# Kernel tuning notes

Measured on AMD Instinct MI355X. Metric: run time of the kernel, lower is better.

The kernel has to match this reference:

```python
import jax, jax.numpy as jnp
import numpy as np

N = 100000
IN_DIM = 128
OUT_DIM = 128
HEADS = 4
C = OUT_DIM // HEADS  # per-head channels = 32
E = 1600000
EPS = 1e-5
NEG_SLOPE = 0.2


def setup_inputs() -> dict:
    key = jax.random.key(0)
    ks = jax.random.split(key, 10)
    prev = jax.random.normal(ks[0], (N, OUT_DIM), dtype=jnp.float32)
    x = jax.random.normal(ks[1], (N, IN_DIM), dtype=jnp.float32)
    edge_index = jax.random.randint(ks[2], (2, E), 0, N, dtype=jnp.int32)
    # GATConv parameters (glorot-ish scale)
    W = jax.random.normal(ks[3], (IN_DIM, HEADS * C), dtype=jnp.float32) * (1.0 / np.sqrt(IN_DIM))
    att_src = jax.random.normal(ks[4], (HEADS, C), dtype=jnp.float32) * (1.0 / np.sqrt(C))
    att_dst = jax.random.normal(ks[5], (HEADS, C), dtype=jnp.float32) * (1.0 / np.sqrt(C))
    bias = jnp.zeros((HEADS * C,), dtype=jnp.float32)
    # BatchNorm1d affine params
    gamma = jnp.ones((OUT_DIM,), dtype=jnp.float32)
    beta = jnp.zeros((OUT_DIM,), dtype=jnp.float32)
    return {"prev": prev, "x": x, "edge_index": edge_index, "W": W,
            "att_src": att_src, "att_dst": att_dst, "bias": bias,
            "gamma": gamma, "beta": beta}


def reference(prev, x, edge_index, W, att_src, att_dst, bias, gamma, beta):
    # --- GATConv (PyG defaults: add_self_loops=True, concat=True, neg_slope=0.2) ---
    n = x.shape[0]
    # add self loops
    loops = jnp.arange(n, dtype=edge_index.dtype)
    src = jnp.concatenate([edge_index[0], loops])  # [E+N] message source j
    dst = jnp.concatenate([edge_index[1], loops])  # [E+N] message target i

    h = (x @ W).reshape(n, HEADS, C)               # [N,H,C]
    a_src = jnp.einsum('nhc,hc->nh', h, att_src)   # [N,H]
    a_dst = jnp.einsum('nhc,hc->nh', h, att_dst)   # [N,H]

    alpha = a_src[src] + a_dst[dst]                # [E',H]
    alpha = jax.nn.leaky_relu(alpha, NEG_SLOPE)
    # segment softmax over incoming edges of each dst node
    amax = jax.ops.segment_max(alpha, dst, num_segments=n)       # [N,H]
    alpha = jnp.exp(alpha - amax[dst])
    asum = jax.ops.segment_sum(alpha, dst, num_segments=n)       # [N,H]
    alpha = alpha / asum[dst]

    msg = h[src] * alpha[:, :, None]                              # [E',H,C]
    out = jax.ops.segment_sum(msg, dst, num_segments=n)          # [N,H,C]
    out = out.reshape(n, HEADS * C) + bias                       # concat heads + bias

    # --- residual + BatchNorm1d (training-mode batch stats) + activation ---
    y = prev + out
    mean = jnp.mean(y, axis=0)
    var = jnp.mean(jnp.square(y - mean), axis=0)  # biased variance (torch BN)
    y = gamma * (y - mean) * jax.lax.rsqrt(var + EPS) + beta
    return jax.nn.relu(y)
```

## Files before the change

kernel.cpp:

```cpp
#include <hip/hip_runtime.h>
#include <math.h>

#define DIM 128
#define NEG 0.2f
#define EPS 1e-5f
#define LOG2E 1.4426950408889634f

#if __has_builtin(__builtin_amdgcn_exp2f)
#define EXP2(x) __builtin_amdgcn_exp2f(x)
#else
#define EXP2(x) exp2f(x)
#endif

typedef __attribute__((ext_vector_type(8))) short short8v;
typedef __attribute__((ext_vector_type(4))) float f32x4;

static __device__ __forceinline__ float leaky(float a) { return a > 0.f ? a : NEG * a; }
static __device__ __forceinline__ float bf2f(unsigned short u) {
    return __uint_as_float(((unsigned int)u) << 16);
}
static __device__ __forceinline__ unsigned short f2bf(float f) {
    unsigned int u = __float_as_uint(f);
    unsigned int r = (u + 0x7fffu + ((u >> 16) & 1u)) >> 16;
    return (unsigned short)r;
}

__global__ __launch_bounds__(256) void k_gemm(const float* __restrict__ x,
                                              const float* __restrict__ W,
                                              const float* __restrict__ att_s,
                                              const float* __restrict__ att_d,
                                              unsigned int* __restrict__ hpk,
                                              float* __restrict__ asrc,
                                              float* __restrict__ adst, int n) {
    __shared__ __align__(16) unsigned short xs[16][136];
    const int tid = threadIdx.x;
    const int w = tid >> 6;
    const int lane = tid & 63;
    const int lm = lane & 15;
    const int lk = lane >> 4;
    short8v bfrag[2][4];
#pragma unroll
    for (int ct = 0; ct < 2; ++ct) {
        int c = w * 32 + ct * 16 + lm;
#pragma unroll
        for (int q = 0; q < 4; ++q) {
            short8v f;
#pragma unroll
            for (int j = 0; j < 8; ++j) {
                int k = q * 32 + lk * 8 + j;
                f[j] = (short)f2bf(W[k * DIM + c]);
            }
            bfrag[ct][q] = f;
        }
    }
    const float asv0 = att_s[w * 32 + lm] * LOG2E;
    const float asv1 = att_s[w * 32 + 16 + lm] * LOG2E;
    const float adv0 = att_d[w * 32 + lm] * LOG2E;
    const float adv1 = att_d[w * 32 + 16 + lm] * LOG2E;

    const int nchunk = (n + 15) >> 4;
    for (int chunk = blockIdx.x; chunk < nchunk; chunk += gridDim.x) {
        const int r0 = chunk * 16;
        {
            int row = tid >> 4;
            int c8 = (tid & 15) * 8;
            int rg = min(r0 + row, n - 1);
            const float4* xp = (const float4*)(x + (size_t)rg * DIM + c8);
            float4 v0 = xp[0], v1 = xp[1];
            short8v t;
            t[0] = (short)f2bf(v0.x); t[1] = (short)f2bf(v0.y);
            t[2] = (short)f2bf(v0.z); t[3] = (short)f2bf(v0.w);
            t[4] = (short)f2bf(v1.x); t[5] = (short)f2bf(v1.y);
            t[6] = (short)f2bf(v1.z); t[7] = (short)f2bf(v1.w);
            *(short8v*)(&xs[row][c8]) = t;
        }
        __syncthreads();
        f32x4 acc0 = {0.f, 0.f, 0.f, 0.f}, acc1 = {0.f, 0.f, 0.f, 0.f};
#pragma unroll
        for (int q = 0; q < 4; ++q) {
            short8v a = *(const short8v*)(&xs[lm][q * 32 + lk * 8]);
            acc0 = __builtin_amdgcn_mfma_f32_16x16x32_bf16(a, bfrag[0][q], acc0, 0, 0, 0);
            acc1 = __builtin_amdgcn_mfma_f32_16x16x32_bf16(a, bfrag[1][q], acc1, 0, 0, 0);
        }
        __syncthreads();
        float ps[4], qs[4];
#pragma unroll
        for (int j = 0; j < 4; ++j) {
            ps[j] = acc0[j] * asv0 + acc1[j] * asv1;
            qs[j] = acc0[j] * adv0 + acc1[j] * adv1;
        }
#pragma unroll
        for (int m = 1; m < 16; m <<= 1) {
#pragma unroll
            for (int j = 0; j < 4; ++j) {
                ps[j] += __shfl_xor(ps[j], m);
                qs[j] += __shfl_xor(qs[j], m);
            }
        }
#pragma unroll
        for (int j = 0; j < 4; ++j) {
            int r = r0 + 4 * lk + j;
            if (r < n) {
                hpk[(size_t)r * 64 + 16 * w + lm] =
                    (unsigned int)f2bf(acc0[j]) | ((unsigned int)f2bf(acc1[j]) << 16);
                if (lm == 0) {
                    asrc[r * 4 + w] = ps[j];
                    adst[r * 4 + w] = qs[j];
                }
            }
        }
    }
}

__global__ void k_init(int* __restrict__ deg, float* __restrict__ stats, int n) {
    int t = blockIdx.x * blockDim.x + threadIdx.x;
    if (t < n) deg[t] = 1;
    if (t < 256) stats[t] = 0.f;
}

__global__ __launch_bounds__(256) void k_hist(const int* __restrict__ dst,
                                              int* __restrict__ deg, int E, int n) {
    const int g = blockIdx.x & 7;
    const int gb = blockIdx.x >> 3;
    const int nblk = gridDim.x >> 3;
    const int wsz = (n + 7) >> 3;
    const int lo = g * wsz;
    const int hi = min(lo + wsz, n);
    const int step = nblk * 256;
    for (int t = gb * 256 + threadIdx.x; t < E; t += step) {
        int d = dst[t];
        if (d >= lo && d < hi) atomicAdd(&deg[d], 1);
    }
}

__global__ __launch_bounds__(256) void k_scan_part(const int* __restrict__ deg,
                                                   int* __restrict__ bsum, int n) {
    int idx = blockIdx.x * 1024 + threadIdx.x * 4;
    int4 v = {0, 0, 0, 0};
    if (idx + 3 < n) v = *(const int4*)(deg + idx);
    else {
        if (idx + 0 < n) v.x = deg[idx + 0];
        if (idx + 1 < n) v.y = deg[idx + 1];
        if (idx + 2 < n) v.z = deg[idx + 2];
    }
    int s = v.x + v.y + v.z + v.w;
#pragma unroll
    for (int m = 1; m < 64; m <<= 1) s += __shfl_xor(s, m);
    __shared__ int ws[4];
    if ((threadIdx.x & 63) == 0) ws[threadIdx.x >> 6] = s;
    __syncthreads();
    if (threadIdx.x == 0) bsum[blockIdx.x] = ws[0] + ws[1] + ws[2] + ws[3];
}

__global__ __launch_bounds__(256) void k_scan_tops(int* __restrict__ bsum, int B) {
    __shared__ int lds[256];
    int t = threadIdx.x;
    int v = (t < B) ? bsum[t] : 0;
    lds[t] = v;
    __syncthreads();
    int acc = v;
    for (int ofs = 1; ofs < 256; ofs <<= 1) {
        int u = (t >= ofs) ? lds[t - ofs] : 0;
        __syncthreads();
        acc += u;
        lds[t] = acc;
        __syncthreads();
    }
    if (t < B) bsum[t] = acc - v;
}

__global__ __launch_bounds__(256) void k_scan_add(const int* __restrict__ deg,
                                                  const int* __restrict__ bsum,
                                                  int* __restrict__ row_start,
                                                  int* __restrict__ cursor, int n, int total) {
    int t = threadIdx.x;
    int idx = blockIdx.x * 1024 + t * 4;
    int4 v = {0, 0, 0, 0};
    if (idx + 3 < n) v = *(const int4*)(deg + idx);
    else {
        if (idx + 0 < n) v.x = deg[idx + 0];
        if (idx + 1 < n) v.y = deg[idx + 1];
        if (idx + 2 < n) v.z = deg[idx + 2];
    }
    int s = v.x + v.y + v.z + v.w;
    __shared__ int lds[256];
    lds[t] = s;
    __syncthreads();
    int acc = s;
    for (int ofs = 1; ofs < 256; ofs <<= 1) {
        int u = (t >= ofs) ? lds[t - ofs] : 0;
        __syncthreads();
        acc += u;
        lds[t] = acc;
        __syncthreads();
    }
    int excl = bsum[blockIdx.x] + acc - s;
    int4 rs;
    rs.x = excl;
    rs.y = rs.x + v.x;
    rs.z = rs.y + v.y;
    rs.w = rs.z + v.z;
    if (idx + 3 < n) {
        *(int4*)(row_start + idx) = rs;
        *(int4*)(cursor + idx) = rs;
    } else {
        if (idx + 0 < n) { row_start[idx + 0] = rs.x; cursor[idx + 0] = rs.x; }
        if (idx + 1 < n) { row_start[idx + 1] = rs.y; cursor[idx + 1] = rs.y; }
        if (idx + 2 < n) { row_start[idx + 2] = rs.z; cursor[idx + 2] = rs.z; }
    }
    if (blockIdx.x == 0 && t == 0) row_start[n] = total;
}

__global__ __launch_bounds__(256) void k_scatter(const int* __restrict__ src,
                                                 const int* __restrict__ dst,
                                                 const float4* __restrict__ asrc4,
                                                 const float4* __restrict__ adst4,
                                                 int* __restrict__ cursor,
                                                 int* __restrict__ csr,
                                                 uint2* __restrict__ pw,
                                                 int E, int n) {
    const int g = blockIdx.x & 7;
    const int gb = blockIdx.x >> 3;
    const int nblk = gridDim.x >> 3;
    const int wsz = (n + 7) >> 3;
    const int lo = g * wsz;
    const int hi = min(lo + wsz, n);
    const int total = E + n;
    const int step = nblk * 256;
    for (int t = gb * 256 + threadIdx.x; t < total; t += step) {
        int d, sv;
        if (t < E) {
            d = dst[t];
            sv = src[t];
        } else {
            d = t - E;
            sv = d;
        }
        if (d >= lo && d < hi) {
            float4 a = asrc4[sv];
            float4 b = adst4[d];
            float p0 = EXP2(leaky(a.x + b.x));
            float p1 = EXP2(leaky(a.y + b.y));
            float p2 = EXP2(leaky(a.z + b.z));
            float p3 = EXP2(leaky(a.w + b.w));
            int slot = atomicAdd(&cursor[d], 1);
            csr[slot] = sv;
            uint2 o;
            o.x = (unsigned int)f2bf(p0) | ((unsigned int)f2bf(p1) << 16);
            o.y = (unsigned int)f2bf(p2) | ((unsigned int)f2bf(p3) << 16);
            pw[slot] = o;
        }
    }
}

__global__ __launch_bounds__(256) void k_agg(const unsigned int* __restrict__ hw,
                                             const unsigned short* __restrict__ pwh,
                                             const int* __restrict__ row_start,
                                             const int* __restrict__ csr,
                                             const float* __restrict__ prev,
                                             const float* __restrict__ bias,
                                             float* __restrict__ ypre,
                                             float* __restrict__ stats, int n) {
    const int lane = threadIdx.x & 63;
    const int hd = lane >> 4;
    const int ch = 32 * hd + (lane & 15);
    int wave = blockIdx.x * 4 + (threadIdx.x >> 6);
    int nw = gridDim.x * 4;
    const float bb0 = bias[ch], bb1 = bias[ch + 16];
    float bsum0 = 0.f, bsq0 = 0.f, bsum1 = 0.f, bsq1 = 0.f;
    for (int i0 = wave; i0 < n; i0 += nw) {
        int i = __builtin_amdgcn_readfirstlane(i0);
        int e0 = row_start[i], e1 = row_start[i + 1];
        float s = 0.f, acc0 = 0.f, acc1 = 0.f;
        for (int e = e0; e < e1; e += 16) {
            int j[16];
            float p[16];
            unsigned int hp[16];
#pragma unroll
            for (int r = 0; r < 16; ++r) {
                int ec = min(e + r, e1 - 1);
                j[r] = csr[ec];
                p[r] = bf2f(pwh[ec * 4 + hd]);
            }
#pragma unroll
            for (int r = 0; r < 16; ++r) hp[r] = hw[(size_t)j[r] * 64 + lane];
#pragma unroll
            for (int r = 0; r < 16; ++r) {
                float pp = (e + r < e1) ? p[r] : 0.f;
                s += pp;
                acc0 = fmaf(pp, __uint_as_float(hp[r] << 16), acc0);
                acc1 = fmaf(pp, __uint_as_float(hp[r] & 0xffff0000u), acc1);
            }
        }
        float rs = 1.0f / s;
        size_t base = (size_t)i * DIM;
        float o0 = fmaf(acc0, rs, bb0 + prev[base + ch]);
        float o1 = fmaf(acc1, rs, bb1 + prev[base + ch + 16]);
        ypre[base + ch] = o0;
        ypre[base + ch + 16] = o1;
        bsum0 += o0; bsq0 = fmaf(o0, o0, bsq0);
        bsum1 += o1; bsq1 = fmaf(o1, o1, bsq1);
    }
    __shared__ float red[4][256];
    red[0][threadIdx.x] = bsum0;
    red[1][threadIdx.x] = bsq0;
    red[2][threadIdx.x] = bsum1;
    red[3][threadIdx.x] = bsq1;
    __syncthreads();
    if (threadIdx.x < 64) {
        int t = threadIdx.x;
        int c = 32 * (t >> 4) + (t & 15);
        float v0 = red[0][t] + red[0][t + 64] + red[0][t + 128] + red[0][t + 192];
        float v1 = red[1][t] + red[1][t + 64] + red[1][t + 128] + red[1][t + 192];
        float v2 = red[2][t] + red[2][t + 64] + red[2][t + 128] + red[2][t + 192];
        float v3 = red[3][t] + red[3][t + 64] + red[3][t + 128] + red[3][t + 192];
        atomicAdd(&stats[c], v0);
        atomicAdd(&stats[c + 16], v2);
        atomicAdd(&stats[128 + c], v1);
        atomicAdd(&stats[128 + c + 16], v3);
    }
}

__global__ void k_bnfin(const float* __restrict__ stats, const float* __restrict__ gamma,
                        const float* __restrict__ beta, float* __restrict__ AB, int n) {
    int c = threadIdx.x;
    float fn = (float)n;
    float mean = stats[c] / fn;
    float var = stats[128 + c] / fn - mean * mean;
    float a = gamma[c] * rsqrtf(var + EPS);
    AB[c] = a;
    AB[128 + c] = beta[c] - mean * a;
}

__global__ __launch_bounds__(256) void k_final(float* __restrict__ y,
                                               const float* __restrict__ AB, int total4) {
    int t0 = blockIdx.x * blockDim.x + threadIdx.x;
    int stride = gridDim.x * blockDim.x;
    for (int t = t0; t < total4; t += stride) {
        float4 v = ((float4*)y)[t];
        int c0 = (t * 4) & 127;
        v.x = fmaf(v.x, AB[c0 + 0], AB[128 + c0 + 0]);
        v.y = fmaf(v.y, AB[c0 + 1], AB[128 + c0 + 1]);
        v.z = fmaf(v.z, AB[c0 + 2], AB[128 + c0 + 2]);
        v.w = fmaf(v.w, AB[c0 + 3], AB[128 + c0 + 3]);
        v.x = v.x > 0.f ? v.x : 0.f;
        v.y = v.y > 0.f ? v.y : 0.f;
        v.z = v.z > 0.f ? v.z : 0.f;
        v.w = v.w > 0.f ? v.w : 0.f;
        ((float4*)y)[t] = v;
    }
}

extern "C" void kernel_launch(void* const* d_in, const int* in_sizes, int n_in,
                              void* d_out, int out_size, void* d_ws, size_t ws_size,
                              hipStream_t stream) {
    const float* prev  = (const float*)d_in[0];
    const float* x     = (const float*)d_in[1];
    const int*   ei    = (const int*)d_in[2];
    const float* W     = (const float*)d_in[3];
    const float* att_s = (const float*)d_in[4];
    const float* att_d = (const float*)d_in[5];
    const float* bias  = (const float*)d_in[6];
    const float* gamma = (const float*)d_in[7];
    const float* beta  = (const float*)d_in[8];
    const int n = in_sizes[0] / DIM;
    const int E = in_sizes[2] / 2;
    const int* src = ei;
    const int* dst = ei + E;

    char* p = (char*)d_ws;
    auto alloc = [&](size_t bytes) {
        void* q = (void*)p;
        p += (bytes + 255) & ~(size_t)255;
        return q;
    };
    unsigned int* hpk = (unsigned int*)alloc((size_t)n * 64 * 4);
    float* asrc      = (float*)alloc((size_t)n * 4 * 4);
    float* adst      = (float*)alloc((size_t)n * 4 * 4);
    int*   deg       = (int*)alloc((size_t)(n + 1) * 4);
    int*   row_start = (int*)alloc((size_t)(n + 1) * 4);
    int*   cursor    = (int*)alloc((size_t)(n + 1) * 4);
    int*   csr       = (int*)alloc((size_t)(E + n + 16) * 4);
    uint2* pw        = (uint2*)alloc((size_t)(E + n + 16) * 8);
    int*   bsum      = (int*)alloc(1024 * 4);
    float* stats     = (float*)alloc(256 * 4);
    float* AB        = (float*)alloc(256 * 4);
    float* yout      = (float*)d_out;

    int B = (n + 1023) / 1024;
    k_init<<<dim3((n + 255) / 256), dim3(256), 0, stream>>>(deg, stats, n);
    k_gemm<<<dim3(1024), dim3(256), 0, stream>>>(x, W, att_s, att_d, hpk, asrc, adst, n);
    k_hist<<<dim3(2048), dim3(256), 0, stream>>>(dst, deg, E, n);
    k_scan_part<<<dim3(B), dim3(256), 0, stream>>>(deg, bsum, n);
    k_scan_tops<<<dim3(1), dim3(256), 0, stream>>>(bsum, B);
    k_scan_add<<<dim3(B), dim3(256), 0, stream>>>(deg, bsum, row_start, cursor, n, E + n);
    k_scatter<<<dim3(2048), dim3(256), 0, stream>>>(src, dst, (const float4*)asrc,
                                                    (const float4*)adst, cursor, csr, pw, E, n);
    k_agg<<<dim3(2048), dim3(256), 0, stream>>>(hpk, (const unsigned short*)pw, row_start,
                                                csr, prev, bias, yout, stats, n);
    k_bnfin<<<dim3(1), dim3(128), 0, stream>>>(stats, gamma, beta, AB, n);
    int total4 = n * DIM / 4;
    k_final<<<dim3(2048), dim3(256), 0, stream>>>(yout, AB, total4);
}
```

Baseline: 307.3 us.

## Gather neighbor rows with 16-byte loads, four edges per wave step

The aggregation kernel now splits each wave into four quarter-waves that each handle a different edge. Each lane loads a uint4 holding eight bf16 channels of the neighbor row, where before every lane loaded one 4-byte word per edge. The goal is fewer, wider gather instructions and more edges in flight per load batch. In exchange it adds a cross-quarter shuffle reduction per node, leaves three quarters of the lanes idle during the output epilogue, and changes the BN stats reduction layout.

```diff
diff --git a/kernel.cpp b/kernel.cpp
--- a/kernel.cpp
+++ b/kernel.cpp
@@ -262,62 +262,89 @@
                                              float* __restrict__ ypre,
                                              float* __restrict__ stats, int n) {
     const int lane = threadIdx.x & 63;
-    const int hd = lane >> 4;
-    const int ch = 32 * hd + (lane & 15);
-    int wave = blockIdx.x * 4 + (threadIdx.x >> 6);
+    const int ql = lane >> 4;
+    const int ll = lane & 15;
+    const int hq = ll >> 2;
+    const int wv = threadIdx.x >> 6;
+    int wave = blockIdx.x * 4 + wv;
     int nw = gridDim.x * 4;
-    const float bb0 = bias[ch], bb1 = bias[ch + 16];
-    float bsum0 = 0.f, bsq0 = 0.f, bsum1 = 0.f, bsq1 = 0.f;
-    for (int i0 = wave; i0 < n; i0 += nw) {
-        int i = __builtin_amdgcn_readfirstlane(i0);
+    float bs_lo[4] = {0.f, 0.f, 0.f, 0.f}, bq_lo[4] = {0.f, 0.f, 0.f, 0.f};
+    float bs_hi[4] = {0.f, 0.f, 0.f, 0.f}, bq_hi[4] = {0.f, 0.f, 0.f, 0.f};
+    for (int i = wave; i < n; i += nw) {
         int e0 = row_start[i], e1 = row_start[i + 1];
-        float s = 0.f, acc0 = 0.f, acc1 = 0.f;
+        float s = 0.f;
+        float ac_lo[4] = {0.f, 0.f, 0.f, 0.f}, ac_hi[4] = {0.f, 0.f, 0.f, 0.f};
         for (int e = e0; e < e1; e += 16) {
-            int j[16];
-            float p[16];
-            unsigned int hp[16];
-#pragma unroll
-            for (int r = 0; r < 16; ++r) {
-                int ec = min(e + r, e1 - 1);
-                j[r] = csr[ec];
-                p[r] = bf2f(pwh[ec * 4 + hd]);
-            }
-#pragma unroll
-            for (int r = 0; r < 16; ++r) hp[r] = hw[(size_t)j[r] * 64 + lane];
-#pragma unroll
-            for (int r = 0; r < 16; ++r) {
-                float pp = (e + r < e1) ? p[r] : 0.f;
-                s += pp;
-                acc0 = fmaf(pp, __uint_as_float(hp[r] << 16), acc0);
-                acc1 = fmaf(pp, __uint_as_float(hp[r] & 0xffff0000u), acc1);
-            }
-        }
-        float rs = 1.0f / s;
-        size_t base = (size_t)i * DIM;
-        float o0 = fmaf(acc0, rs, bb0 + prev[base + ch]);
-        float o1 = fmaf(acc1, rs, bb1 + prev[base + ch + 16]);
-        ypre[base + ch] = o0;
-        ypre[base + ch + 16] = o1;
-        bsum0 += o0; bsq0 = fmaf(o0, o0, bsq0);
-        bsum1 += o1; bsq1 = fmaf(o1, o1, bsq1);
-    }
-    __shared__ float red[4][256];
-    red[0][threadIdx.x] = bsum0;
-    red[1][threadIdx.x] = bsq0;
-    red[2][threadIdx.x] = bsum1;
-    red[3][threadIdx.x] = bsq1;
+            int j[4];
+            float pp[4];
+            uint4 hv[4];
+#pragma unroll
+            for (int b = 0; b < 4; ++b) {
+                int ee = e + b * 4 + ql;
+                int ec = min(ee, e1 - 1);
+                j[b] = csr[ec];
+                pp[b] = (ee < e1) ? bf2f(pwh[ec * 4 + hq]) : 0.f;
+            }
+#pragma unroll
+            for (int b = 0; b < 4; ++b)
+                hv[b] = ((const uint4*)(hw + (size_t)j[b] * 64))[ll];
+#pragma unroll
+            for (int b = 0; b < 4; ++b) {
+                s += pp[b];
+                unsigned int h0 = hv[b].x, h1 = hv[b].y, h2 = hv[b].z, h3 = hv[b].w;
+                ac_lo[0] = fmaf(pp[b], __uint_as_float(h0 << 16), ac_lo[0]);
+                ac_hi[0] = fmaf(pp[b], __uint_as_float(h0 & 0xffff0000u), ac_hi[0]);
+                ac_lo[1] = fmaf(pp[b], __uint_as_float(h1 << 16), ac_lo[1]);
+                ac_hi[1] = fmaf(pp[b], __uint_as_float(h1 & 0xffff0000u), ac_hi[1]);
+                ac_lo[2] = fmaf(pp[b], __uint_as_float(h2 << 16), ac_lo[2]);
+                ac_hi[2] = fmaf(pp[b], __uint_as_float(h2 & 0xffff0000u), ac_hi[2]);
+                ac_lo[3] = fmaf(pp[b], __uint_as_float(h3 << 16), ac_lo[3]);
+                ac_hi[3] = fmaf(pp[b], __uint_as_float(h3 & 0xffff0000u), ac_hi[3]);
+            }
+        }
+#pragma unroll
+        for (int m = 16; m < 64; m <<= 1) {
+            s += __shfl_xor(s, m);
+#pragma unroll
+            for (int u = 0; u < 4; ++u) {
+                ac_lo[u] += __shfl_xor(ac_lo[u], m);
+                ac_hi[u] += __shfl_xor(ac_hi[u], m);
+            }
+        }
+        if (ql == 0) {
+            float rs = 1.0f / s;
+            size_t base = (size_t)i * DIM;
+#pragma unroll
+            for (int u = 0; u < 4; ++u) {
+                int ug = ll * 4 + u;
+                int c = 32 * (ug >> 4) + (ug & 15);
+                float o_lo = fmaf(ac_lo[u], rs, bias[c] + prev[base + c]);
+                float o_hi = fmaf(ac_hi[u], rs, bias[c + 16] + prev[base + c + 16]);
+                ypre[base + c] = o_lo;
+                ypre[base + c + 16] = o_hi;
+                bs_lo[u] += o_lo; bq_lo[u] = fmaf(o_lo, o_lo, bq_lo[u]);
+                bs_hi[u] += o_hi; bq_hi[u] = fmaf(o_hi, o_hi, bq_hi[u]);
+            }
+        }
+    }
+    __shared__ float rsum[128][4];
+    __shared__ float rsq[128][4];
+    if (ql == 0) {
+#pragma unroll
+        for (int u = 0; u < 4; ++u) {
+            int ug = ll * 4 + u;
+            int c = 32 * (ug >> 4) + (ug & 15);
+            rsum[c][wv] = bs_lo[u];
+            rsum[c + 16][wv] = bs_hi[u];
+            rsq[c][wv] = bq_lo[u];
+            rsq[c + 16][wv] = bq_hi[u];
+        }
+    }
     __syncthreads();
-    if (threadIdx.x < 64) {
-        int t = threadIdx.x;
-        int c = 32 * (t >> 4) + (t & 15);
-        float v0 = red[0][t] + red[0][t + 64] + red[0][t + 128] + red[0][t + 192];
-        float v1 = red[1][t] + red[1][t + 64] + red[1][t + 128] + red[1][t + 192];
-        float v2 = red[2][t] + red[2][t + 64] + red[2][t + 128] + red[2][t + 192];
-        float v3 = red[3][t] + red[3][t + 64] + red[3][t + 128] + red[3][t + 192];
-        atomicAdd(&stats[c], v0);
-        atomicAdd(&stats[c + 16], v2);
-        atomicAdd(&stats[128 + c], v1);
-        atomicAdd(&stats[128 + c + 16], v3);
+    if (threadIdx.x < 128) {
+        int c = threadIdx.x;
+        atomicAdd(&stats[c], rsum[c][0] + rsum[c][1] + rsum[c][2] + rsum[c][3]);
+        atomicAdd(&stats[128 + c], rsq[c][0] + rsq[c][1] + rsq[c][2] + rsq[c][3]);
     }
 }
 
```

Result: slower. 324.6 us (+5.6%).
